# Kernel optimization log

Hardware: AMD Instinct MI355X
Metric: run time of the kernel (lower is better)

## Reference

```python
import jax, jax.numpy as jnp
import numpy as np

EMB = 1024
HEADS = 16
HEAD_DIM = EMB // HEADS


def setup_inputs() -> dict:
    key = jax.random.key(0)
    ks = jax.random.split(key, 9)
    B, T = 2, 2048
    s = 1.0 / np.sqrt(EMB)
    x = jax.random.normal(ks[0], (B, T, EMB), dtype=jnp.float32)
    Wq = jax.random.normal(ks[1], (EMB, EMB), dtype=jnp.float32) * s
    bq = jnp.zeros((EMB,), dtype=jnp.float32)
    Wk = jax.random.normal(ks[2], (EMB, EMB), dtype=jnp.float32) * s
    bk = jnp.zeros((EMB,), dtype=jnp.float32)
    Wv = jax.random.normal(ks[3], (EMB, EMB), dtype=jnp.float32) * s
    bv = jnp.zeros((EMB,), dtype=jnp.float32)
    Wo = jax.random.normal(ks[4], (EMB, EMB), dtype=jnp.float32) * s
    bo = jnp.zeros((EMB,), dtype=jnp.float32)
    return {"x": x, "Wq": Wq, "bq": bq, "Wk": Wk, "bk": bk,
            "Wv": Wv, "bv": bv, "Wo": Wo, "bo": bo}


def reference(x, Wq, bq, Wk, bk, Wv, bv, Wo, bo):
    B, T, C = x.shape
    H, D = HEADS, HEAD_DIM
    # QKV projections -> (B, H, T, D)
    q = (x @ Wq + bq).reshape(B, T, H, D).transpose(0, 2, 1, 3)
    k = (x @ Wk + bk).reshape(B, T, H, D).transpose(0, 2, 1, 3)
    v = (x @ Wv + bv).reshape(B, T, H, D).transpose(0, 2, 1, 3)
    scores = jnp.einsum('bhqd,bhkd->bhqk', q, k) / np.sqrt(D).astype(np.float32)
    causal = jnp.tril(jnp.ones((T, T), dtype=bool))  # True where allowed
    scores = jnp.where(causal, scores, -jnp.inf)
    weights = jax.nn.softmax(scores, axis=-1)  # dropout is identity at eval
    out = jnp.einsum('bhqk,bhkd->bhqd', weights, v)
    out = out.transpose(0, 2, 1, 3).reshape(B, T, C)
    return out @ Wo + bo
```

## Files before the change

### kernel.cpp

```cpp
#include <hip/hip_runtime.h>

typedef unsigned short u16;
typedef u16 u16x8 __attribute__((ext_vector_type(8)));
typedef __bf16 bf16x8 __attribute__((ext_vector_type(8)));
typedef float f32x4 __attribute__((ext_vector_type(4)));

#define EMB 1024
#define TT 2048
#define BB 2
#define NHEADS 16
#define HD 64
#define MTOT (BB * TT)

__device__ __forceinline__ u16 cvt(float f) {
  return __builtin_bit_cast(u16, (__bf16)f);
}

__device__ __forceinline__ bf16x8 asbf(u16x8 v) {
  return __builtin_bit_cast(bf16x8, v);
}

__device__ __forceinline__ void gload16(const void* g, void* l) {
  __builtin_amdgcn_global_load_lds(
      (const __attribute__((address_space(1))) void*)g,
      (__attribute__((address_space(3))) void*)l, 16, 0, 0);
}

__global__ __launch_bounds__(256) void k_prep(
    const float* __restrict__ x, u16* __restrict__ xb,
    const float* __restrict__ W0, const float* __restrict__ W1,
    const float* __restrict__ W2, const float* __restrict__ W3,
    u16* __restrict__ T0, u16* __restrict__ T1, u16* __restrict__ T2,
    u16* __restrict__ T3) {
  __shared__ float tile[32][33];
  const int bid = blockIdx.x;
  const int tid = threadIdx.x;
  if (bid >= 4096) {
    int i = (bid - 4096) * 256 + tid;
    float4 a = ((const float4*)x)[i * 2];
    float4 b = ((const float4*)x)[i * 2 + 1];
    u16x8 o;
    o[0] = cvt(a.x); o[1] = cvt(a.y); o[2] = cvt(a.z); o[3] = cvt(a.w);
    o[4] = cvt(b.x); o[5] = cvt(b.y); o[6] = cvt(b.z); o[7] = cvt(b.w);
    ((u16x8*)xb)[i] = o;
    return;
  }
  const int z = bid >> 10;
  const float* __restrict__ W = (z == 0) ? W0 : (z == 1) ? W1 : (z == 2) ? W2 : W3;
  u16* __restrict__ Wt = (z == 0) ? T0 : (z == 1) ? T1 : (z == 2) ? T2 : T3;
  const int b = bid & 1023;
  const int bx = (b & 31) * 32, by = (b >> 5) * 32;
  const int tx = tid & 31;
  const int ty = tid >> 5;
#pragma unroll
  for (int r = ty; r < 32; r += 8) tile[r][tx] = W[(by + r) * EMB + bx + tx];
  __syncthreads();
#pragma unroll
  for (int r = ty; r < 32; r += 8)
    Wt[(bx + r) * EMB + by + tx] = cvt(tile[tx][r]);
}

__global__ __launch_bounds__(256) void k_gemm_qkv(
    const u16* __restrict__ xb, const u16* __restrict__ WqT,
    const u16* __restrict__ WkT, const u16* __restrict__ WvT,
    const float* __restrict__ bq, const float* __restrict__ bk,
    const float* __restrict__ bv, u16* __restrict__ Q, u16* __restrict__ K,
    u16* __restrict__ Vt) {
  __shared__ u16 Al[128 * 32];
  __shared__ u16 Bl[128 * 32];
  const int tid = threadIdx.x;
  const int lane = tid & 63;
  const int w = tid >> 6;
  const int wr = w >> 1, wc = w & 1;
  const int lr = lane & 15, lg = lane >> 4;
  const int wg = blockIdx.y * 32 + blockIdx.x;
  const int swz = (wg & 7) * 96 + (wg >> 3);
  const int m0 = (swz & 31) * 128;
  const int nb = swz >> 5;
  const int seg = nb >> 3;
  const int n0 = (nb & 7) * 128;
  const u16* __restrict__ Bt = (seg == 0) ? WqT : (seg == 1) ? WkT : WvT;
  const float* __restrict__ bias = (seg == 0) ? bq : (seg == 1) ? bk : bv;

  f32x4 acc[4][4];
#pragma unroll
  for (int i = 0; i < 4; i++)
#pragma unroll
    for (int j = 0; j < 4; j++) acc[i][j] = (f32x4){0.f, 0.f, 0.f, 0.f};

  const int srow = tid >> 2;
  const int scol = (tid & 3) * 8;
  const u16* ga0 = xb + (m0 + srow) * EMB + scol;
  const u16* gb0 = Bt + (n0 + srow) * EMB + scol;
  char* la0 = (char*)Al + w * 1024;
  char* lb0 = (char*)Bl + w * 1024;

  for (int k0 = 0; k0 < EMB; k0 += 32) {
    gload16(ga0 + k0, la0);
    gload16(ga0 + 64 * EMB + k0, la0 + 4096);
    gload16(gb0 + k0, lb0);
    gload16(gb0 + 64 * EMB + k0, lb0 + 4096);
    __syncthreads();
    u16x8 af[4], bfr[4];
#pragma unroll
    for (int mi = 0; mi < 4; mi++)
      af[mi] = *(const u16x8*)&Al[(wr * 64 + mi * 16 + lr) * 32 + lg * 8];
#pragma unroll
    for (int ni = 0; ni < 4; ni++)
      bfr[ni] = *(const u16x8*)&Bl[(wc * 64 + ni * 16 + lr) * 32 + lg * 8];
#pragma unroll
    for (int mi = 0; mi < 4; mi++)
#pragma unroll
      for (int ni = 0; ni < 4; ni++)
        acc[mi][ni] = __builtin_amdgcn_mfma_f32_16x16x32_bf16(
            asbf(af[mi]), asbf(bfr[ni]), acc[mi][ni], 0, 0, 0);
    __syncthreads();
  }

#pragma unroll
  for (int mi = 0; mi < 4; mi++) {
    const int lmb = wr * 64 + mi * 16 + lg * 4;
#pragma unroll
    for (int ni = 0; ni < 4; ni++) {
      const int ln = wc * 64 + ni * 16 + lr;
      const int n = n0 + ln;
      const float bv_ = bias[n];
      const int h = n >> 6, d = n & 63;
#pragma unroll
      for (int r = 0; r < 4; r++) {
        const int m = m0 + lmb + r;
        const int b = m >> 11, t = m & 2047;
        float v = acc[mi][ni][r] + bv_;
        if (seg == 0) {
          v *= 0.18033688011f;
          Q[(((b * NHEADS + h) * TT) + t) * HD + d] = cvt(v);
        } else if (seg == 1) {
          K[(((b * NHEADS + h) * TT) + t) * HD + d] = cvt(v);
        } else {
          Vt[(((b * NHEADS + h) * HD) + d) * TT + t] = cvt(v);
        }
      }
    }
  }
}

__global__ __launch_bounds__(512) void k_attn(const u16* __restrict__ Q,
                                              const u16* __restrict__ Kg,
                                              const u16* __restrict__ Vt,
                                              u16* __restrict__ AO) {
  __shared__ u16 Kl[2][64 * 64];
  __shared__ u16 Vl[2][64 * 64];
  __shared__ u16 Plds[8][16][68];
  const int tid = threadIdx.x;
  const int lane = tid & 63;
  const int w = tid >> 6;
  const int lr = lane & 15, lg = lane >> 4;
  const int bh = blockIdx.x;
  const int pair = blockIdx.y;
  const int lo = pair, hi = 31 - pair;
  const int qblk = (w < 4) ? hi : lo;
  const int myend = qblk;
  const int q0 = qblk * 64 + (w & 3) * 16;
  const u16* __restrict__ Qh = Q + bh * TT * HD;
  const u16* __restrict__ Kh = Kg + bh * TT * HD;
  const u16* __restrict__ Vh = Vt + bh * HD * TT;

  const int srow = tid >> 3;
  const int sc = (tid & 7) ^ (srow & 7);

  u16x8 qf[2];
  qf[0] = *(const u16x8*)&Qh[(q0 + lr) * HD + lg * 8];
  qf[1] = *(const u16x8*)&Qh[(q0 + lr) * HD + 32 + lg * 8];

  f32x4 accO[4];
#pragma unroll
  for (int i = 0; i < 4; i++) accO[i] = (f32x4){0.f, 0.f, 0.f, 0.f};
  float mst[4] = {-__builtin_inff(), -__builtin_inff(), -__builtin_inff(),
                  -__builtin_inff()};
  float lsum[4] = {0.f, 0.f, 0.f, 0.f};

  const int nkt = hi + 1;

  gload16(Kh + srow * HD + sc * 8, (char*)Kl[0] + w * 1024);
  gload16(Vh + srow * TT + 0 + sc * 8, (char*)Vl[0] + w * 1024);
  __syncthreads();

  for (int kt = 0; kt < nkt; ++kt) {
    const int k0 = kt * 64;
    const int cur = kt & 1;
    if (kt + 1 < nkt) {
      const int kn = k0 + 64;
      gload16(Kh + (kn + srow) * HD + sc * 8, (char*)Kl[cur ^ 1] + w * 1024);
      gload16(Vh + srow * TT + kn + sc * 8, (char*)Vl[cur ^ 1] + w * 1024);
    }
    if (kt <= myend) {
      const char* Kc = (const char*)Kl[cur];
      const char* Vc = (const char*)Vl[cur];

      f32x4 s[4];
#pragma unroll
      for (int n = 0; n < 4; n++) s[n] = (f32x4){0.f, 0.f, 0.f, 0.f};
      __builtin_amdgcn_s_setprio(1);
#pragma unroll
      for (int n = 0; n < 4; n++) {
        const int row = n * 16 + lr;
#pragma unroll
        for (int dh = 0; dh < 2; dh++) {
          const int bo = (dh * 64 + lg * 16) ^ ((row & 7) << 4);
          u16x8 kf = *(const u16x8*)(Kc + row * 128 + bo);
          s[n] = __builtin_amdgcn_mfma_f32_16x16x32_bf16(asbf(qf[dh]),
                                                         asbf(kf), s[n], 0, 0, 0);
        }
      }
      __builtin_amdgcn_s_setprio(0);
      if (kt == myend) {
#pragma unroll
        for (int n = 0; n < 4; n++)
#pragma unroll
          for (int r = 0; r < 4; r++) {
            int col = k0 + n * 16 + lr, row = q0 + lg * 4 + r;
            if (col > row) s[n][r] = -__builtin_inff();
          }
      }
      float lmax[4];
#pragma unroll
      for (int r = 0; r < 4; r++)
        lmax[r] = fmaxf(fmaxf(s[0][r], s[1][r]), fmaxf(s[2][r], s[3][r]));
      float g0 = fmaxf(lmax[0] - mst[0], lmax[1] - mst[1]);
      float g1 = fmaxf(lmax[2] - mst[2], lmax[3] - mst[3]);
      if (!__all(fmaxf(g0, g1) <= 11.0f)) {
#pragma unroll
        for (int r = 0; r < 4; r++) {
          float rm = lmax[r];
          rm = fmaxf(rm, __shfl_xor(rm, 1, 16));
          rm = fmaxf(rm, __shfl_xor(rm, 2, 16));
          rm = fmaxf(rm, __shfl_xor(rm, 4, 16));
          rm = fmaxf(rm, __shfl_xor(rm, 8, 16));
          float mnew = fmaxf(mst[r], rm);
          float corr = exp2f(mst[r] - mnew);
          lsum[r] *= corr;
          mst[r] = mnew;
#pragma unroll
          for (int dt = 0; dt < 4; dt++) accO[dt][r] *= corr;
        }
      }
#pragma unroll
      for (int r = 0; r < 4; r++) {
        float p0 = exp2f(s[0][r] - mst[r]);
        float p1 = exp2f(s[1][r] - mst[r]);
        float p2 = exp2f(s[2][r] - mst[r]);
        float p3 = exp2f(s[3][r] - mst[r]);
        lsum[r] += (p0 + p1) + (p2 + p3);
        const int row = lg * 4 + r;
        Plds[w][row][lr] = cvt(p0);
        Plds[w][row][16 + lr] = cvt(p1);
        Plds[w][row][32 + lr] = cvt(p2);
        Plds[w][row][48 + lr] = cvt(p3);
      }
      u16x8 pa0 = *(const u16x8*)&Plds[w][lr][lg * 8];
      u16x8 pa1 = *(const u16x8*)&Plds[w][lr][32 + lg * 8];
      __builtin_amdgcn_s_setprio(1);
#pragma unroll
      for (int dt = 0; dt < 4; dt++) {
        const int row = dt * 16 + lr;
        const int bo0 = (lg * 16) ^ ((row & 7) << 4);
        const int bo1 = (64 + lg * 16) ^ ((row & 7) << 4);
        u16x8 vf0 = *(const u16x8*)(Vc + row * 128 + bo0);
        u16x8 vf1 = *(const u16x8*)(Vc + row * 128 + bo1);
        accO[dt] = __builtin_amdgcn_mfma_f32_16x16x32_bf16(asbf(pa0),
                                                           asbf(vf0), accO[dt], 0, 0, 0);
        accO[dt] = __builtin_amdgcn_mfma_f32_16x16x32_bf16(asbf(pa1),
                                                           asbf(vf1), accO[dt], 0, 0, 0);
      }
      __builtin_amdgcn_s_setprio(0);
    }
    __syncthreads();
  }
  float rinv[4];
#pragma unroll
  for (int r = 0; r < 4; r++) {
    float t = lsum[r];
    t += __shfl_xor(t, 1, 16);
    t += __shfl_xor(t, 2, 16);
    t += __shfl_xor(t, 4, 16);
    t += __shfl_xor(t, 8, 16);
    rinv[r] = 1.0f / t;
  }
  const int b = bh >> 4, h = bh & 15;
#pragma unroll
  for (int dt = 0; dt < 4; dt++)
#pragma unroll
    for (int r = 0; r < 4; r++) {
      const int row = q0 + lg * 4 + r;
      const int d = h * 64 + dt * 16 + lr;
      AO[(b * TT + row) * EMB + d] = cvt(accO[dt][r] * rinv[r]);
    }
}

__global__ __launch_bounds__(256) void k_gemm_out(const u16* __restrict__ AO,
                                                  const u16* __restrict__ WoT,
                                                  const float* __restrict__ bo,
                                                  float* __restrict__ out) {
  __shared__ u16 Al[128 * 32];
  __shared__ u16 Bl[128 * 32];
  const int tid = threadIdx.x;
  const int lane = tid & 63;
  const int w = tid >> 6;
  const int wr = w >> 1, wc = w & 1;
  const int lr = lane & 15, lg = lane >> 4;
  const int wg = blockIdx.y * 32 + blockIdx.x;
  const int swz = (wg & 7) * 32 + (wg >> 3);
  const int m0 = (swz & 31) * 128;
  const int n0 = (swz >> 5) * 128;

  f32x4 acc[4][4];
#pragma unroll
  for (int i = 0; i < 4; i++)
#pragma unroll
    for (int j = 0; j < 4; j++) acc[i][j] = (f32x4){0.f, 0.f, 0.f, 0.f};

  const int srow = tid >> 2;
  const int scol = (tid & 3) * 8;
  const u16* ga0 = AO + (m0 + srow) * EMB + scol;
  const u16* gb0 = WoT + (n0 + srow) * EMB + scol;
  char* la0 = (char*)Al + w * 1024;
  char* lb0 = (char*)Bl + w * 1024;

  for (int k0 = 0; k0 < EMB; k0 += 32) {
    gload16(ga0 + k0, la0);
    gload16(ga0 + 64 * EMB + k0, la0 + 4096);
    gload16(gb0 + k0, lb0);
    gload16(gb0 + 64 * EMB + k0, lb0 + 4096);
    __syncthreads();
    u16x8 af[4], bfr[4];
#pragma unroll
    for (int mi = 0; mi < 4; mi++)
      af[mi] = *(const u16x8*)&Al[(wr * 64 + mi * 16 + lr) * 32 + lg * 8];
#pragma unroll
    for (int ni = 0; ni < 4; ni++)
      bfr[ni] = *(const u16x8*)&Bl[(wc * 64 + ni * 16 + lr) * 32 + lg * 8];
#pragma unroll
    for (int mi = 0; mi < 4; mi++)
#pragma unroll
      for (int ni = 0; ni < 4; ni++)
        acc[mi][ni] = __builtin_amdgcn_mfma_f32_16x16x32_bf16(
            asbf(af[mi]), asbf(bfr[ni]), acc[mi][ni], 0, 0, 0);
    __syncthreads();
  }

#pragma unroll
  for (int mi = 0; mi < 4; mi++) {
    const int lmb = wr * 64 + mi * 16 + lg * 4;
#pragma unroll
    for (int ni = 0; ni < 4; ni++) {
      const int ln = wc * 64 + ni * 16 + lr;
      const int n = n0 + ln;
      const float bv_ = bo[n];
#pragma unroll
      for (int r = 0; r < 4; r++) {
        const int m = m0 + lmb + r;
        out[m * EMB + n] = acc[mi][ni][r] + bv_;
      }
    }
  }
}

extern "C" void kernel_launch(void* const* d_in, const int* in_sizes, int n_in,
                              void* d_out, int out_size, void* d_ws,
                              size_t ws_size, hipStream_t stream) {
  const float* x = (const float*)d_in[0];
  const float* Wq = (const float*)d_in[1];
  const float* bq = (const float*)d_in[2];
  const float* Wk = (const float*)d_in[3];
  const float* bk = (const float*)d_in[4];
  const float* Wv = (const float*)d_in[5];
  const float* bv = (const float*)d_in[6];
  const float* Wo = (const float*)d_in[7];
  const float* bo = (const float*)d_in[8];
  float* out = (float*)d_out;

  char* ws = (char*)d_ws;
  u16* xb = (u16*)ws;
  u16* WqT = (u16*)(ws + (8u << 20));
  u16* WkT = (u16*)(ws + (10u << 20));
  u16* WvT = (u16*)(ws + (12u << 20));
  u16* WoT = (u16*)(ws + (14u << 20));
  u16* Qb = (u16*)(ws + (16u << 20));
  u16* Kb = (u16*)(ws + (24u << 20));
  u16* Vtb = (u16*)(ws + (32u << 20));
  u16* AO = xb;

  k_prep<<<6144, 256, 0, stream>>>(x, xb, Wq, Wk, Wv, Wo, WqT, WkT, WvT, WoT);
  k_gemm_qkv<<<dim3(32, 24), 256, 0, stream>>>(xb, WqT, WkT, WvT, bq, bk, bv,
                                               Qb, Kb, Vtb);
  k_attn<<<dim3(32, 16), 512, 0, stream>>>(Qb, Kb, Vtb, AO);
  k_gemm_out<<<dim3(32, 8), 256, 0, stream>>>(AO, WoT, bo, out);
}
```

Measured before the change: 136.4 us.

## Compute transposed S in attention to keep P in registers, drop GEMM swizzle

```diff
diff --git a/kernel.cpp b/kernel.cpp
--- a/kernel.cpp
+++ b/kernel.cpp
@@ -73,10 +73,8 @@
   const int w = tid >> 6;
   const int wr = w >> 1, wc = w & 1;
   const int lr = lane & 15, lg = lane >> 4;
-  const int wg = blockIdx.y * 32 + blockIdx.x;
-  const int swz = (wg & 7) * 96 + (wg >> 3);
-  const int m0 = (swz & 31) * 128;
-  const int nb = swz >> 5;
+  const int m0 = blockIdx.x * 128;
+  const int nb = blockIdx.y;
   const int seg = nb >> 3;
   const int n0 = (nb & 7) * 128;
   const u16* __restrict__ Bt = (seg == 0) ? WqT : (seg == 1) ? WkT : WvT;
@@ -150,7 +148,6 @@
                                               u16* __restrict__ AO) {
   __shared__ u16 Kl[2][64 * 64];
   __shared__ u16 Vl[2][64 * 64];
-  __shared__ u16 Plds[8][16][68];
   const int tid = threadIdx.x;
   const int lane = tid & 63;
   const int w = tid >> 6;
@@ -166,7 +163,8 @@
   const u16* __restrict__ Vh = Vt + bh * HD * TT;
 
   const int srow = tid >> 3;
-  const int sc = (tid & 7) ^ (srow & 7);
+  const int sgz = ((tid >> 3) & 3) | (((tid >> 6) & 1) << 2);
+  const int sc = (tid & 7) ^ sgz;
 
   u16x8 qf[2];
   qf[0] = *(const u16x8*)&Qh[(q0 + lr) * HD + lg * 8];
@@ -175,14 +173,13 @@
   f32x4 accO[4];
 #pragma unroll
   for (int i = 0; i < 4; i++) accO[i] = (f32x4){0.f, 0.f, 0.f, 0.f};
-  float mst[4] = {-__builtin_inff(), -__builtin_inff(), -__builtin_inff(),
-                  -__builtin_inff()};
-  float lsum[4] = {0.f, 0.f, 0.f, 0.f};
+  float mst = -__builtin_inff();
+  float lsum = 0.f;
 
   const int nkt = hi + 1;
 
   gload16(Kh + srow * HD + sc * 8, (char*)Kl[0] + w * 1024);
-  gload16(Vh + srow * TT + 0 + sc * 8, (char*)Vl[0] + w * 1024);
+  gload16(Vh + srow * TT + sc * 8, (char*)Vl[0] + w * 1024);
   __syncthreads();
 
   for (int kt = 0; kt < nkt; ++kt) {
@@ -203,89 +200,91 @@
       __builtin_amdgcn_s_setprio(1);
 #pragma unroll
       for (int n = 0; n < 4; n++) {
-        const int row = n * 16 + lr;
+        const int kr =
+            (lr & 3) + ((n & 1) << 2) + ((lr >> 2) << 3) + ((n >> 1) << 5);
+        const int gg = (kr & 3) | (((kr >> 3) & 1) << 2);
 #pragma unroll
         for (int dh = 0; dh < 2; dh++) {
-          const int bo = (dh * 64 + lg * 16) ^ ((row & 7) << 4);
-          u16x8 kf = *(const u16x8*)(Kc + row * 128 + bo);
-          s[n] = __builtin_amdgcn_mfma_f32_16x16x32_bf16(asbf(qf[dh]),
-                                                         asbf(kf), s[n], 0, 0, 0);
+          const int bo = ((dh * 4 + lg) ^ gg) << 4;
+          u16x8 kf = *(const u16x8*)(Kc + kr * 128 + bo);
+          s[n] = __builtin_amdgcn_mfma_f32_16x16x32_bf16(asbf(kf), asbf(qf[dh]),
+                                                         s[n], 0, 0, 0);
         }
       }
       __builtin_amdgcn_s_setprio(0);
       if (kt == myend) {
-#pragma unroll
-        for (int n = 0; n < 4; n++)
-#pragma unroll
-          for (int r = 0; r < 4; r++) {
-            int col = k0 + n * 16 + lr, row = q0 + lg * 4 + r;
-            if (col > row) s[n][r] = -__builtin_inff();
-          }
-      }
-      float lmax[4];
-#pragma unroll
-      for (int r = 0; r < 4; r++)
-        lmax[r] = fmaxf(fmaxf(s[0][r], s[1][r]), fmaxf(s[2][r], s[3][r]));
-      float g0 = fmaxf(lmax[0] - mst[0], lmax[1] - mst[1]);
-      float g1 = fmaxf(lmax[2] - mst[2], lmax[3] - mst[3]);
-      if (!__all(fmaxf(g0, g1) <= 11.0f)) {
+        const int rowq = q0 + lr;
+#pragma unroll
+        for (int n = 0; n < 4; n++) {
+          const int cb = k0 + ((n & 1) << 2) + (lg << 3) + ((n >> 1) << 5);
+#pragma unroll
+          for (int r = 0; r < 4; r++)
+            if (cb + r > rowq) s[n][r] = -__builtin_inff();
+        }
+      }
+      float m01 = fmaxf(fmaxf(s[0][0], s[0][1]), fmaxf(s[0][2], s[0][3]));
+      float m1 = fmaxf(fmaxf(s[1][0], s[1][1]), fmaxf(s[1][2], s[1][3]));
+      float m2 = fmaxf(fmaxf(s[2][0], s[2][1]), fmaxf(s[2][2], s[2][3]));
+      float m3 = fmaxf(fmaxf(s[3][0], s[3][1]), fmaxf(s[3][2], s[3][3]));
+      float lmax = fmaxf(fmaxf(m01, m1), fmaxf(m2, m3));
+      if (!__all(lmax - mst <= 11.0f)) {
+        float rm = lmax;
+        rm = fmaxf(rm, __shfl_xor(rm, 16));
+        rm = fmaxf(rm, __shfl_xor(rm, 32));
+        float mnew = fmaxf(mst, rm);
+        float corr = exp2f(mst - mnew);
+        lsum *= corr;
+        mst = mnew;
 #pragma unroll
         for (int r = 0; r < 4; r++) {
-          float rm = lmax[r];
-          rm = fmaxf(rm, __shfl_xor(rm, 1, 16));
-          rm = fmaxf(rm, __shfl_xor(rm, 2, 16));
-          rm = fmaxf(rm, __shfl_xor(rm, 4, 16));
-          rm = fmaxf(rm, __shfl_xor(rm, 8, 16));
-          float mnew = fmaxf(mst[r], rm);
-          float corr = exp2f(mst[r] - mnew);
-          lsum[r] *= corr;
-          mst[r] = mnew;
-#pragma unroll
-          for (int dt = 0; dt < 4; dt++) accO[dt][r] *= corr;
-        }
-      }
+          float ca = __shfl(corr, 20 * lg + r);
+#pragma unroll
+          for (int dt = 0; dt < 4; dt++) accO[dt][r] *= ca;
+        }
+      }
+      float p[4][4];
+      float ls = 0.f;
+#pragma unroll
+      for (int n = 0; n < 4; n++)
+#pragma unroll
+        for (int r = 0; r < 4; r++) {
+          p[n][r] = exp2f(s[n][r] - mst);
+          ls += p[n][r];
+        }
+      lsum += ls;
+      u16x8 a1, a2;
 #pragma unroll
       for (int r = 0; r < 4; r++) {
-        float p0 = exp2f(s[0][r] - mst[r]);
-        float p1 = exp2f(s[1][r] - mst[r]);
-        float p2 = exp2f(s[2][r] - mst[r]);
-        float p3 = exp2f(s[3][r] - mst[r]);
-        lsum[r] += (p0 + p1) + (p2 + p3);
-        const int row = lg * 4 + r;
-        Plds[w][row][lr] = cvt(p0);
-        Plds[w][row][16 + lr] = cvt(p1);
-        Plds[w][row][32 + lr] = cvt(p2);
-        Plds[w][row][48 + lr] = cvt(p3);
-      }
-      u16x8 pa0 = *(const u16x8*)&Plds[w][lr][lg * 8];
-      u16x8 pa1 = *(const u16x8*)&Plds[w][lr][32 + lg * 8];
+        a1[r] = cvt(p[0][r]);
+        a1[4 + r] = cvt(p[1][r]);
+        a2[r] = cvt(p[2][r]);
+        a2[4 + r] = cvt(p[3][r]);
+      }
       __builtin_amdgcn_s_setprio(1);
 #pragma unroll
       for (int dt = 0; dt < 4; dt++) {
         const int row = dt * 16 + lr;
-        const int bo0 = (lg * 16) ^ ((row & 7) << 4);
-        const int bo1 = (64 + lg * 16) ^ ((row & 7) << 4);
+        const int gg = (row & 3) | (((row >> 3) & 1) << 2);
+        const int bo0 = ((lg ^ gg) << 4);
+        const int bo1 = (((4 + lg) ^ gg) << 4);
         u16x8 vf0 = *(const u16x8*)(Vc + row * 128 + bo0);
         u16x8 vf1 = *(const u16x8*)(Vc + row * 128 + bo1);
-        accO[dt] = __builtin_amdgcn_mfma_f32_16x16x32_bf16(asbf(pa0),
-                                                           asbf(vf0), accO[dt], 0, 0, 0);
-        accO[dt] = __builtin_amdgcn_mfma_f32_16x16x32_bf16(asbf(pa1),
-                                                           asbf(vf1), accO[dt], 0, 0, 0);
+        accO[dt] = __builtin_amdgcn_mfma_f32_16x16x32_bf16(asbf(a1), asbf(vf0),
+                                                           accO[dt], 0, 0, 0);
+        accO[dt] = __builtin_amdgcn_mfma_f32_16x16x32_bf16(asbf(a2), asbf(vf1),
+                                                           accO[dt], 0, 0, 0);
       }
       __builtin_amdgcn_s_setprio(0);
     }
     __syncthreads();
   }
-  float rinv[4];
-#pragma unroll
-  for (int r = 0; r < 4; r++) {
-    float t = lsum[r];
-    t += __shfl_xor(t, 1, 16);
-    t += __shfl_xor(t, 2, 16);
-    t += __shfl_xor(t, 4, 16);
-    t += __shfl_xor(t, 8, 16);
-    rinv[r] = 1.0f / t;
-  }
+  float t = lsum;
+  t += __shfl_xor(t, 16);
+  t += __shfl_xor(t, 32);
+  float rinv = 1.0f / t;
+  float ra[4];
+#pragma unroll
+  for (int r = 0; r < 4; r++) ra[r] = __shfl(rinv, 20 * lg + r);
   const int b = bh >> 4, h = bh & 15;
 #pragma unroll
   for (int dt = 0; dt < 4; dt++)
@@ -293,7 +292,7 @@
     for (int r = 0; r < 4; r++) {
       const int row = q0 + lg * 4 + r;
       const int d = h * 64 + dt * 16 + lr;
-      AO[(b * TT + row) * EMB + d] = cvt(accO[dt][r] * rinv[r]);
+      AO[(b * TT + row) * EMB + d] = cvt(accO[dt][r] * ra[r]);
     }
 }
 
@@ -308,10 +307,8 @@
   const int w = tid >> 6;
   const int wr = w >> 1, wc = w & 1;
   const int lr = lane & 15, lg = lane >> 4;
-  const int wg = blockIdx.y * 32 + blockIdx.x;
-  const int swz = (wg & 7) * 32 + (wg >> 3);
-  const int m0 = (swz & 31) * 128;
-  const int n0 = (swz >> 5) * 128;
+  const int m0 = blockIdx.x * 128;
+  const int n0 = blockIdx.y * 128;
 
   f32x4 acc[4][4];
 #pragma unroll
```

Result: faster. 114.7 us (-15.9%).
